# Performance work log

Hardware: AMD Instinct MI355X
Metric: run time of the kernel (lower is better)

Reference implementation:

```python
import jax, jax.numpy as jnp
import numpy as np

C = 512
G = 32  # GroupNorm groups
EPS = 1e-6


def setup_inputs() -> dict:
    key = jax.random.key(0)
    ks = jax.random.split(key, 12)
    B, H, W = 2, 64, 64
    s = 0.02
    return {
        "x": jax.random.normal(ks[0], (B, C, H, W), dtype=jnp.float32),
        "gn_w": jnp.ones((C,), jnp.float32),
        "gn_b": jnp.zeros((C,), jnp.float32),
        "wq": jax.random.normal(ks[1], (C, C), jnp.float32) * s,
        "bq": jnp.zeros((C,), jnp.float32),
        "wk": jax.random.normal(ks[2], (C, C), jnp.float32) * s,
        "bk": jnp.zeros((C,), jnp.float32),
        "wv": jax.random.normal(ks[3], (C, C), jnp.float32) * s,
        "bv": jnp.zeros((C,), jnp.float32),
        "wp": jax.random.normal(ks[4], (C, C), jnp.float32) * s,
        "bp": jnp.zeros((C,), jnp.float32),
    }


def _group_norm(x, w, b):
    B, Cc, H, W = x.shape
    xg = x.reshape(B, G, Cc // G, H, W)
    mu = jnp.mean(xg, axis=(2, 3, 4), keepdims=True)
    var = jnp.var(xg, axis=(2, 3, 4), keepdims=True)
    xn = ((xg - mu) * jax.lax.rsqrt(var + EPS)).reshape(B, Cc, H, W)
    return xn * w[None, :, None, None] + b[None, :, None, None]


def reference(x, gn_w, gn_b, wq, bq, wk, bk, wv, bv, wp, bp):
    B, Cc, H, W = x.shape
    N = H * W
    h = _group_norm(x, gn_w, gn_b)
    hf = h.reshape(B, Cc, N)  # [B,C,N]
    # 1x1 conv == per-position linear over channels
    q = jnp.einsum('dc,bcn->bdn', wq, hf) + bq[None, :, None]
    k = jnp.einsum('dc,bcn->bdn', wk, hf) + bk[None, :, None]
    v = jnp.einsum('dc,bcn->bdn', wv, hf) + bv[None, :, None]
    scale = float(Cc) ** -0.5
    # scores[b,q_pos,k_pos]
    w_ = jnp.einsum('bcq,bck->bqk', q, k) * scale
    w_ = jax.nn.softmax(w_, axis=2)
    # h_[b,c,q] = sum_k v[b,c,k] * w_[b,q,k]
    o = jnp.einsum('bck,bqk->bcq', v, w_)
    o = jnp.einsum('dc,bcn->bdn', wp, o) + bp[None, :, None]
    return x + o.reshape(B, Cc, H, W)
```

## Files before the change

### kernel.cpp

```cpp
#include <hip/hip_runtime.h>


typedef unsigned short u16;
typedef unsigned int u32;
typedef unsigned char u8;
typedef float f32x4 __attribute__((ext_vector_type(4)));

#define NPOS 4096
#define CCH 512

__device__ __forceinline__ u16 f2bf(float f) {
  u32 u = __builtin_bit_cast(u32, f);
  u += 0x7fffu + ((u >> 16) & 1u);
  return (u16)(u >> 16);
}
__device__ __forceinline__ float bf2f(u16 h) {
  u32 u = ((u32)h) << 16;
  return __builtin_bit_cast(float, u);
}
__device__ __forceinline__ u8 f2fp8(float f) {
  u32 pk = __builtin_amdgcn_cvt_pk_fp8_f32(f, f, 0, false);
  return (u8)(pk & 0xff);
}

__device__ __forceinline__ void load16_lds8(const u8* g, u8* l) {
  __builtin_amdgcn_global_load_lds(
      (const __attribute__((address_space(1))) void*)g,
      (__attribute__((address_space(3))) void*)l, 16, 0, 0);
}

__global__ __launch_bounds__(256) void gn_stats_part(const float* __restrict__ x,
                                                     float2* __restrict__ part) {
  int id = blockIdx.x;
  const float4* p = (const float4*)(x + (size_t)id * 16384);
  float s = 0.f, s2 = 0.f;
  for (int i = threadIdx.x; i < 4096; i += 256) {
    float4 u = p[i];
    s += u.x + u.y + u.z + u.w;
    s2 += u.x * u.x + u.y * u.y + u.z * u.z + u.w * u.w;
  }
  for (int o = 32; o; o >>= 1) {
    s += __shfl_xor(s, o);
    s2 += __shfl_xor(s2, o);
  }
  __shared__ float rs[4], rq[4];
  int lane = threadIdx.x & 63, w = threadIdx.x >> 6;
  if (lane == 0) { rs[w] = s; rq[w] = s2; }
  __syncthreads();
  if (threadIdx.x == 0)
    part[id] = make_float2(rs[0] + rs[1] + rs[2] + rs[3], rq[0] + rq[1] + rq[2] + rq[3]);
}

__global__ __launch_bounds__(256) void gn_apply8(const float* __restrict__ x,
                                                 const float* __restrict__ gnw,
                                                 const float* __restrict__ gnb,
                                                 const float2* __restrict__ pstats,
                                                 u8* __restrict__ h8) {
  int b = blockIdx.z, c0 = blockIdx.y * 64, n0 = blockIdx.x * 64;
  __shared__ u8 lt[64][80];
  const float* xb = x + (size_t)b * CCH * NPOS;
  int tid = threadIdx.x;
#pragma unroll
  for (int it = 0; it < 4; ++it) {
    int ci = (tid >> 4) + it * 16;
    int nj = (tid & 15) * 4;
    int c = c0 + ci;
    float4 v = *(const float4*)&xb[(size_t)c * NPOS + n0 + nj];
    const float2* pp = pstats + ((size_t)b * 32 + (c >> 4)) * 4;
    float s = pp[0].x + pp[1].x + pp[2].x + pp[3].x;
    float s2 = pp[0].y + pp[1].y + pp[2].y + pp[3].y;
    float mu = s * (1.f / 65536.f);
    float var = s2 * (1.f / 65536.f) - mu * mu;
    float rst = rsqrtf(var + 1e-6f);
    float w = gnw[c] * rst;
    float bb = gnb[c] - mu * w;
    lt[nj + 0][ci] = f2fp8(v.x * w + bb);
    lt[nj + 1][ci] = f2fp8(v.y * w + bb);
    lt[nj + 2][ci] = f2fp8(v.z * w + bb);
    lt[nj + 3][ci] = f2fp8(v.w * w + bb);
  }
  __syncthreads();
  int ni = tid >> 2, cj = (tid & 3) * 16;
  uint4 o = *(const uint4*)&lt[ni][cj];
  *(uint4*)&h8[((size_t)b * NPOS + n0 + ni) * CCH + c0 + cj] = o;
}

__global__ __launch_bounds__(256) void wconv8(const float* __restrict__ w0,
                                              const float* __restrict__ w1,
                                              const float* __restrict__ w2,
                                              const float* __restrict__ w3,
                                              u8* __restrict__ dst,
                                              const float* __restrict__ bq,
                                              const float* __restrict__ bk,
                                              const float* __restrict__ bv,
                                              float* __restrict__ bqkv) {
  int which = blockIdx.y;
  int bx = blockIdx.x;
  int t = threadIdx.x;
  if (bx == 256) {
    if (which < 3) {
      const float* bsrc = which == 0 ? bq : which == 1 ? bk : bv;
      bqkv[which * 512 + t] = bsrc[t];
      bqkv[which * 512 + 256 + t] = bsrc[256 + t];
    }
    return;
  }
  const float* src = which == 0 ? w0 : which == 1 ? w1 : which == 2 ? w2 : w3;
  u8* d = dst + (size_t)which * (CCH * CCH);
  int i = bx * 256 + t;
  float4 v = ((const float4*)src)[i];
  u32 pk = __builtin_amdgcn_cvt_pk_fp8_f32(v.x, v.y, 0, false);
  pk = __builtin_amdgcn_cvt_pk_fp8_f32(v.z, v.w, pk, true);
  ((u32*)d)[i] = pk;
}

template <int EPI, bool SWIZ>
__global__ __launch_bounds__(256, 4) void gemm_f8(const u8* __restrict__ A,
                                                  const u8* __restrict__ Bm,
                                                  void* __restrict__ Cv,
                                                  const float* __restrict__ bias,
                                                  const float* __restrict__ resid,
                                                  float* __restrict__ lpart,
                                                  float alpha, int K,
                                                  int lda, int ldb, int ldc,
                                                  long sA, long sB, long sC, long sR) {
  const int b = blockIdx.z;
  int bx = blockIdx.x, by = blockIdx.y;
  if (SWIZ) {
    int id = by * gridDim.x + bx;
    int g = id >> 8;
    int w = id & 255;
    bx = (g << 3) | (w & 7);
    by = w >> 3;
  }
  A += (size_t)b * sA;
  Bm += (size_t)b * sB;
  const int m0 = by * 128, n0 = bx * 128;
  __shared__ u8 sAt[128 * 128];
  __shared__ u8 sBt[128 * 128];
  const int tid = threadIdx.x, wave = tid >> 6, lane = tid & 63;
  const int lrow = lane & 15, kch = lane >> 4;
  const int wm = (wave >> 1) * 64, wn = (wave & 1) * 64;
  const int srow = lane >> 3;
  const int sseg = ((lane & 7) ^ srow) * 16;
  f32x4 acc[4][4] = {};

  for (int k0 = 0; k0 < K; k0 += 128) {
#pragma unroll
    for (int r = 0; r < 4; ++r) {
      int ch = wave * 4 + r;
      load16_lds8(A + (size_t)(m0 + ch * 8 + srow) * lda + (k0 + sseg), sAt + ch * 1024);
      load16_lds8(Bm + (size_t)(n0 + ch * 8 + srow) * ldb + (k0 + sseg), sBt + ch * 1024);
    }
    __syncthreads();
#pragma unroll
    for (int kk = 0; kk < 4; ++kk) {
      const int seg16 = kk * 2 + (kch >> 1);
      const int sub = (kch & 1) * 8;
      long af[4], bf[4];
#pragma unroll
      for (int i = 0; i < 4; ++i) {
        int ra = wm + i * 16 + lrow;
        af[i] = *(const long*)(sAt + ra * 128 + (seg16 ^ (ra & 7)) * 16 + sub);
        int rb = wn + i * 16 + lrow;
        bf[i] = *(const long*)(sBt + rb * 128 + (seg16 ^ (rb & 7)) * 16 + sub);
      }
#pragma unroll
      for (int i = 0; i < 4; ++i)
#pragma unroll
        for (int j = 0; j < 4; ++j)
          acc[i][j] =
              __builtin_amdgcn_mfma_f32_16x16x32_fp8_fp8(af[i], bf[j], acc[i][j], 0, 0, 0);
    }
    __syncthreads();
  }

  const int col = lane & 15, rbase = (lane >> 4) * 4;
  const size_t cb = (size_t)b * sC;
  float rsum[4][4];
  if (EPI == 2) {
#pragma unroll
    for (int i = 0; i < 4; ++i)
#pragma unroll
      for (int r = 0; r < 4; ++r) rsum[i][r] = 0.f;
  }
#pragma unroll
  for (int i = 0; i < 4; ++i) {
    int mrow = m0 + wm + i * 16 + rbase;
#pragma unroll
    for (int j = 0; j < 4; ++j) {
      int ncol = n0 + wn + j * 16 + col;
      float bcol = (EPI == 0) ? bias[ncol] : 0.f;
#pragma unroll
      for (int r = 0; r < 4; ++r) {
        int m = mrow + r;
        size_t ci = cb + (size_t)m * ldc + ncol;
        float v = acc[i][j][r];
        if (EPI == 0) {
          ((u8*)Cv)[ci] = f2fp8(v + bcol);
        } else if (EPI == 1) {
          v = v * alpha + bias[m] + resid[(size_t)b * sR + (size_t)m * ldc + ncol];
          ((float*)Cv)[ci] = v;
        } else {
          float s = fminf(fmaxf(v * alpha, -10.f), 4.5f);
          float e = __expf(s);
          rsum[i][r] += e;
          ((u8*)Cv)[ci] = f2fp8(4.f * e);
        }
      }
    }
  }
  if (EPI == 2) {
#pragma unroll
    for (int i = 0; i < 4; ++i) {
#pragma unroll
      for (int r = 0; r < 4; ++r) {
        float v = rsum[i][r];
        v += __shfl_xor(v, 1);
        v += __shfl_xor(v, 2);
        v += __shfl_xor(v, 4);
        v += __shfl_xor(v, 8);
        if ((lane & 15) == 0) {
          int m = m0 + wm + i * 16 + rbase + r;
          lpart[((size_t)b * NPOS + m) * 64 + bx * 2 + (wave & 1)] = v;
        }
      }
    }
  }
}

__global__ __launch_bounds__(256, 4) void gemm_pv_fp8(const u8* __restrict__ Um,
                                                      const u8* __restrict__ Vm,
                                                      u16* __restrict__ part,
                                                      const float* __restrict__ lpart,
                                                      float* __restrict__ lsum) {
  const int b = blockIdx.z >> 2, slice = blockIdx.z & 3;
  const int id = blockIdx.x + (blockIdx.y << 2);
  const int xcd = id & 7, j = id >> 3;
  const int bx = j & 3, by = xcd + ((j >> 2) << 3);
  const u8* A = Um + (size_t)b * ((size_t)NPOS * NPOS) + (size_t)slice * 1024;
  const u8* Bv = Vm + (size_t)b * (CCH * NPOS) + (size_t)slice * 1024;
  const int m0 = by * 128, n0 = bx * 128;
  __shared__ u8 sA[128 * 128];
  __shared__ u8 sB[128 * 128];
  const int tid = threadIdx.x, wave = tid >> 6, lane = tid & 63;
  const int lrow = lane & 15, kch = lane >> 4;
  const int wm = (wave >> 1) * 64, wn = (wave & 1) * 64;
  const int srow = lane >> 3;
  const int sseg = ((lane & 7) ^ srow) * 16;
  f32x4 acc[4][4] = {};

  for (int k0 = 0; k0 < 1024; k0 += 128) {
#pragma unroll
    for (int r = 0; r < 4; ++r) {
      int ch = wave * 4 + r;
      load16_lds8(A + (size_t)(m0 + ch * 8 + srow) * NPOS + (k0 + sseg), sA + ch * 1024);
      load16_lds8(Bv + (size_t)(n0 + ch * 8 + srow) * NPOS + (k0 + sseg), sB + ch * 1024);
    }
    __syncthreads();
#pragma unroll
    for (int kk = 0; kk < 4; ++kk) {
      const int seg16 = kk * 2 + (kch >> 1);
      const int sub = (kch & 1) * 8;
      long af[4], bf[4];
#pragma unroll
      for (int i = 0; i < 4; ++i) {
        int ra = wm + i * 16 + lrow;
        af[i] = *(const long*)(sA + ra * 128 + (seg16 ^ (ra & 7)) * 16 + sub);
        int rb = wn + i * 16 + lrow;
        bf[i] = *(const long*)(sB + rb * 128 + (seg16 ^ (rb & 7)) * 16 + sub);
      }
#pragma unroll
      for (int i = 0; i < 4; ++i)
#pragma unroll
        for (int jj = 0; jj < 4; ++jj)
          acc[i][jj] =
              __builtin_amdgcn_mfma_f32_16x16x32_fp8_fp8(af[i], bf[jj], acc[i][jj], 0, 0, 0);
    }
    __syncthreads();
  }

  const int col = lane & 15, rbase = (lane >> 4) * 4;
  u16* dst = part + (size_t)slice * ((size_t)2 * NPOS * CCH) + (size_t)b * (NPOS * CCH);
#pragma unroll
  for (int i = 0; i < 4; ++i) {
    int mrow = m0 + wm + i * 16 + rbase;
#pragma unroll
    for (int jj = 0; jj < 4; ++jj) {
      int ncol = n0 + wn + jj * 16 + col;
#pragma unroll
      for (int r = 0; r < 4; ++r)
        dst[(size_t)(mrow + r) * CCH + ncol] = f2bf(acc[i][jj][r]);
    }
  }
  if (bx == 0 && tid < 128) {
    const float* lp = lpart + ((size_t)b * NPOS + m0 + tid) * 64;
    float s = 0.f;
#pragma unroll
    for (int c = 0; c < 64; ++c) s += lp[c];
    lsum[(size_t)b * NPOS + m0 + tid] = s;
  }
}

__global__ __launch_bounds__(256) void merge_pv8(const u16* __restrict__ part,
                                                 const float* __restrict__ lsum,
                                                 u8* __restrict__ dst) {
  const long sl = 4194304;
  int i = blockIdx.x * 256 + threadIdx.x;
  long e0 = (long)i * 8;
  int q = (int)((e0 >> 9) & 4095);
  int b = (int)(e0 >> 21);
  float inv = 8.f / lsum[(size_t)b * NPOS + q];
  uint4 a = ((const uint4*)part)[i];
  uint4 bb = ((const uint4*)(part + sl))[i];
  uint4 c = ((const uint4*)(part + 2 * sl))[i];
  uint4 d = ((const uint4*)(part + 3 * sl))[i];
  u32 wa[4] = {a.x, a.y, a.z, a.w}, wb_[4] = {bb.x, bb.y, bb.z, bb.w};
  u32 wc[4] = {c.x, c.y, c.z, c.w}, wd[4] = {d.x, d.y, d.z, d.w};
  float v[8];
#pragma unroll
  for (int j = 0; j < 4; ++j) {
    v[2 * j] = (bf2f((u16)(wa[j] & 0xffff)) + bf2f((u16)(wb_[j] & 0xffff)) +
                bf2f((u16)(wc[j] & 0xffff)) + bf2f((u16)(wd[j] & 0xffff))) * inv;
    v[2 * j + 1] = (bf2f((u16)(wa[j] >> 16)) + bf2f((u16)(wb_[j] >> 16)) +
                    bf2f((u16)(wc[j] >> 16)) + bf2f((u16)(wd[j] >> 16))) * inv;
  }
  uint2 o;
  u32 p0 = __builtin_amdgcn_cvt_pk_fp8_f32(v[0], v[1], 0, false);
  p0 = __builtin_amdgcn_cvt_pk_fp8_f32(v[2], v[3], p0, true);
  u32 p1 = __builtin_amdgcn_cvt_pk_fp8_f32(v[4], v[5], 0, false);
  p1 = __builtin_amdgcn_cvt_pk_fp8_f32(v[6], v[7], p1, true);
  o.x = p0;
  o.y = p1;
  ((uint2*)dst)[i] = o;
}

__global__ __launch_bounds__(256) void transpose_v8(const u8* __restrict__ src,
                                                    u8* __restrict__ dst, int srcld) {
  int b = blockIdx.z, n0 = blockIdx.x * 64, d0 = blockIdx.y * 64;
  __shared__ u8 lt[64][80];
  const u8* s = src + (size_t)b * NPOS * srcld;
  u8* d = dst + (size_t)b * CCH * NPOS;
  int t = threadIdx.x;
  {
    int r = t >> 2, c16 = (t & 3) * 16;
    uint4 v = *(const uint4*)&s[(size_t)(n0 + r) * srcld + d0 + c16];
    *(uint4*)&lt[r][c16] = v;
  }
  __syncthreads();
  {
    int dr = t >> 2, c16 = (t & 3) * 16;
    u8 tmp[16];
#pragma unroll
    for (int j = 0; j < 16; ++j) tmp[j] = lt[c16 + j][dr];
    *(uint4*)&d[(size_t)(d0 + dr) * NPOS + n0 + c16] = *(uint4*)tmp;
  }
}

extern "C" void kernel_launch(void* const* d_in, const int* in_sizes, int n_in,
                              void* d_out, int out_size, void* d_ws, size_t ws_size,
                              hipStream_t stream) {
  const float* x = (const float*)d_in[0];
  const float* gnw = (const float*)d_in[1];
  const float* gnb = (const float*)d_in[2];
  const float* wq = (const float*)d_in[3];
  const float* bq = (const float*)d_in[4];
  const float* wk = (const float*)d_in[5];
  const float* bk = (const float*)d_in[6];
  const float* wv = (const float*)d_in[7];
  const float* bv = (const float*)d_in[8];
  const float* wp = (const float*)d_in[9];
  const float* bp = (const float*)d_in[10];
  float* out = (float*)d_out;

  char* ws = (char*)d_ws;
  size_t off = 0;
  auto alloc = [&](size_t bytes) {
    void* p = ws + off;
    off += (bytes + 1023) & ~(size_t)1023;
    return p;
  };
  float2* pstats = (float2*)alloc(256 * sizeof(float2));
  u8* w8 = (u8*)alloc((size_t)4 * CCH * CCH);
  u8* wp8 = w8 + 3 * CCH * CCH;
  float* bqkv = (float*)alloc(1536 * sizeof(float));
  u8* h8 = (u8*)alloc((size_t)2 * NPOS * CCH);
  u8* qkv8 = (u8*)alloc((size_t)2 * NPOS * 1536);
  u8* v8 = (u8*)alloc((size_t)2 * CCH * NPOS);
  u8* U8 = (u8*)alloc((size_t)2 * NPOS * NPOS);
  float* lpart = (float*)alloc((size_t)2 * NPOS * 64 * 4);
  float* lsum = (float*)alloc((size_t)2 * NPOS * 4);
  u16* part_pv = (u16*)alloc((size_t)4 * 2 * NPOS * CCH * 2);
  u8* o8 = (u8*)alloc((size_t)2 * NPOS * CCH);

  const long sHC8 = (long)NPOS * CCH;
  const long sQKV8 = (long)NPOS * 1536;
  const long sSS8 = (long)NPOS * NPOS;
  const long sOUT = (long)CCH * NPOS;
  const float scale = 0.044194173824159216f;

  gn_stats_part<<<256, 256, 0, stream>>>(x, pstats);
  gn_apply8<<<dim3(64, 8, 2), 256, 0, stream>>>(x, gnw, gnb, pstats, h8);
  wconv8<<<dim3(257, 4), 256, 0, stream>>>(wq, wk, wv, wp, w8, bq, bk, bv, bqkv);
  gemm_f8<0, false><<<dim3(12, 32, 2), 256, 0, stream>>>(
      h8, w8, qkv8, bqkv, nullptr, nullptr, 1.f, CCH, CCH, CCH, 1536,
      sHC8, 0, sQKV8, 0);
  transpose_v8<<<dim3(64, 8, 2), 256, 0, stream>>>(qkv8 + 1024, v8, 1536);
  gemm_f8<2, true><<<dim3(32, 32, 2), 256, 0, stream>>>(
      qkv8, qkv8 + 512, U8, nullptr, nullptr, lpart, scale, CCH, 1536, 1536, NPOS,
      sQKV8, sQKV8, sSS8, 0);
  gemm_pv_fp8<<<dim3(4, 32, 8), 256, 0, stream>>>(U8, v8, part_pv, lpart, lsum);
  merge_pv8<<<2048, 256, 0, stream>>>(part_pv, lsum, o8);
  gemm_f8<1, false><<<dim3(32, 4, 2), 256, 0, stream>>>(
      wp8, o8, out, bp, x, nullptr, 1.f / 32.f, CCH, CCH, CCH, NPOS,
      0, sHC8, sOUT, sOUT);
}
```

Before: 195.6 us.

## Replace QKV, score and PV GEMMs with 256x256 tiled, 4-stage pipelined kernel

Adds a templated 512-thread GEMM with 256x256 output tiles, a 4-deep LDS ring buffer filled by direct-to-LDS loads with explicit vmcnt waits, XCD-aware block remapping and MFMA priority raising. It is used for the QKV projection, the QK^T exp-score GEMM (with lpart now split into 4 column parts per 256 block) and the split-K PV GEMM. This cuts the number of barriers per k-step, raises data reuse per loaded byte and overlaps global loads with MFMA work. In exchange it uses far more registers and LDS per block, which lowers occupancy, and gives fewer blocks for the small QKV GEMM (192 blocks).

Measured after the change: 214.8 us. 9.8% more time.

```diff
diff --git a/kernel.cpp b/kernel.cpp
--- a/kernel.cpp
+++ b/kernel.cpp
@@ -177,13 +177,6 @@
 
   const int col = lane & 15, rbase = (lane >> 4) * 4;
   const size_t cb = (size_t)b * sC;
-  float rsum[4][4];
-  if (EPI == 2) {
-#pragma unroll
-    for (int i = 0; i < 4; ++i)
-#pragma unroll
-      for (int r = 0; r < 4; ++r) rsum[i][r] = 0.f;
-  }
 #pragma unroll
   for (int i = 0; i < 4; ++i) {
     int mrow = m0 + wm + i * 16 + rbase;
@@ -198,107 +191,168 @@
         float v = acc[i][j][r];
         if (EPI == 0) {
           ((u8*)Cv)[ci] = f2fp8(v + bcol);
-        } else if (EPI == 1) {
+        } else {
           v = v * alpha + bias[m] + resid[(size_t)b * sR + (size_t)m * ldc + ncol];
           ((float*)Cv)[ci] = v;
-        } else {
-          float s = fminf(fmaxf(v * alpha, -10.f), 4.5f);
+        }
+      }
+    }
+  }
+}
+
+template <int EPI, int NT>
+__global__ __launch_bounds__(512, 2) void gemm256(
+    const u8* __restrict__ A, const u8* __restrict__ Bm, void* __restrict__ Cv,
+    const float* __restrict__ bias, float* __restrict__ lpart,
+    const float* __restrict__ lpart_in, float* __restrict__ lsum,
+    float alpha, long lda, long ldb, long ldc, long sA, long sB, long sC) {
+  __shared__ u8 LDS[4][32768];
+
+  int lin = blockIdx.x + gridDim.x * blockIdx.y;
+  const int nq = (gridDim.x * gridDim.y) >> 3;
+  lin = (lin & 7) * nq + (lin >> 3);
+  const int bx = lin % gridDim.x, by = lin / gridDim.x;
+  const int m0 = by * 256, n0 = bx * 256;
+
+  int b;
+  const u8 *Ab, *Bb;
+  if constexpr (EPI == 3) {
+    b = blockIdx.z >> 2;
+    const int slice = blockIdx.z & 3;
+    Ab = A + (size_t)b * sA + (size_t)slice * 1024;
+    Bb = Bm + (size_t)b * sB + (size_t)slice * 1024;
+  } else {
+    b = blockIdx.z;
+    Ab = A + (size_t)b * sA;
+    Bb = Bm + (size_t)b * sB;
+  }
+
+  const int tid = threadIdx.x, wave = tid >> 6, lane = tid & 63;
+  const int lrow = lane & 15, kch = lane >> 4;
+  const int wr = wave >> 2, wc = wave & 3;
+
+  const int srow = wave * 16 + (lane >> 2);
+  const int ssw = ((lane & 3) ^ ((srow >> 1) & 3)) * 16;
+  const u8* gA = Ab + (size_t)(m0 + srow) * lda + ssw;
+  const u8* gB = Bb + (size_t)(n0 + srow) * ldb + ssw;
+  u8* lA = &LDS[0][0] + wave * 1024;
+
+  const int swz = (lrow >> 1) & 3;
+  const int cst = (kch & 1) * 8 + (((kch >> 1) ^ swz) << 4);
+  int aoff[8], boff[4];
+#pragma unroll
+  for (int i = 0; i < 8; ++i) aoff[i] = (wr * 128 + i * 16 + lrow) * 64 + cst;
+#pragma unroll
+  for (int j = 0; j < 4; ++j) boff[j] = (wc * 64 + j * 16 + lrow) * 64 + cst + 16384;
+
+  f32x4 acc[8][4] = {};
+
+  auto STAGE = [&](int t) {
+    const int sl = (t & 3) * 32768;
+    const long k0 = (long)t * 64;
+    load16_lds8(gA + k0, lA + sl);
+    load16_lds8(gB + k0, lA + sl + 16384);
+    load16_lds8(gA + 128 * lda + k0, lA + sl + 8192);
+    load16_lds8(gB + 128 * ldb + k0, lA + sl + 24576);
+  };
+
+  STAGE(0);
+  STAGE(1);
+  STAGE(2);
+
+  for (int t = 0; t < NT; ++t) {
+    if (t < NT - 2)
+      asm volatile("s_waitcnt vmcnt(8)" ::: "memory");
+    else if (t == NT - 2)
+      asm volatile("s_waitcnt vmcnt(4)" ::: "memory");
+    else
+      asm volatile("s_waitcnt vmcnt(0)" ::: "memory");
+    asm volatile("s_barrier" ::: "memory");
+    if (t + 3 < NT) STAGE(t + 3);
+    const u8* sb = &LDS[t & 3][0];
+#pragma unroll
+    for (int g = 0; g < 2; ++g) {
+      long a_[8], b_[4];
+#pragma unroll
+      for (int i = 0; i < 8; ++i) a_[i] = *(const long*)(sb + (aoff[i] ^ (g << 5)));
+#pragma unroll
+      for (int j = 0; j < 4; ++j) b_[j] = *(const long*)(sb + (boff[j] ^ (g << 5)));
+      __builtin_amdgcn_s_setprio(1);
+#pragma unroll
+      for (int i = 0; i < 8; ++i)
+#pragma unroll
+        for (int j = 0; j < 4; ++j)
+          acc[i][j] =
+              __builtin_amdgcn_mfma_f32_16x16x32_fp8_fp8(a_[i], b_[j], acc[i][j], 0, 0, 0);
+      __builtin_amdgcn_s_setprio(0);
+    }
+  }
+
+  const int col = lane & 15, rbase = kch * 4;
+  if constexpr (EPI == 0) {
+    u8* C = (u8*)Cv + (size_t)b * sC;
+#pragma unroll
+    for (int i = 0; i < 8; ++i) {
+      const int mrow = m0 + wr * 128 + i * 16 + rbase;
+#pragma unroll
+      for (int j = 0; j < 4; ++j) {
+        const int ncol = n0 + wc * 64 + j * 16 + col;
+        const float bc = bias[ncol];
+#pragma unroll
+        for (int r = 0; r < 4; ++r)
+          C[(size_t)(mrow + r) * ldc + ncol] = f2fp8(acc[i][j][r] + bc);
+      }
+    }
+  } else if constexpr (EPI == 2) {
+    u8* C = (u8*)Cv + (size_t)b * sC;
+#pragma unroll
+    for (int i = 0; i < 8; ++i) {
+      const int mrow = m0 + wr * 128 + i * 16 + rbase;
+      float rsum[4] = {0.f, 0.f, 0.f, 0.f};
+#pragma unroll
+      for (int j = 0; j < 4; ++j) {
+        const int ncol = n0 + wc * 64 + j * 16 + col;
+#pragma unroll
+        for (int r = 0; r < 4; ++r) {
+          float s = fminf(fmaxf(acc[i][j][r] * alpha, -10.f), 4.5f);
           float e = __expf(s);
-          rsum[i][r] += e;
-          ((u8*)Cv)[ci] = f2fp8(4.f * e);
+          rsum[r] += e;
+          C[(size_t)(mrow + r) * ldc + ncol] = f2fp8(4.f * e);
         }
       }
-    }
-  }
-  if (EPI == 2) {
-#pragma unroll
-    for (int i = 0; i < 4; ++i) {
 #pragma unroll
       for (int r = 0; r < 4; ++r) {
-        float v = rsum[i][r];
+        float v = rsum[r];
         v += __shfl_xor(v, 1);
         v += __shfl_xor(v, 2);
         v += __shfl_xor(v, 4);
         v += __shfl_xor(v, 8);
-        if ((lane & 15) == 0) {
-          int m = m0 + wm + i * 16 + rbase + r;
-          lpart[((size_t)b * NPOS + m) * 64 + bx * 2 + (wave & 1)] = v;
-        }
-      }
-    }
-  }
-}
-
-__global__ __launch_bounds__(256, 4) void gemm_pv_fp8(const u8* __restrict__ Um,
-                                                      const u8* __restrict__ Vm,
-                                                      u16* __restrict__ part,
-                                                      const float* __restrict__ lpart,
-                                                      float* __restrict__ lsum) {
-  const int b = blockIdx.z >> 2, slice = blockIdx.z & 3;
-  const int id = blockIdx.x + (blockIdx.y << 2);
-  const int xcd = id & 7, j = id >> 3;
-  const int bx = j & 3, by = xcd + ((j >> 2) << 3);
-  const u8* A = Um + (size_t)b * ((size_t)NPOS * NPOS) + (size_t)slice * 1024;
-  const u8* Bv = Vm + (size_t)b * (CCH * NPOS) + (size_t)slice * 1024;
-  const int m0 = by * 128, n0 = bx * 128;
-  __shared__ u8 sA[128 * 128];
-  __shared__ u8 sB[128 * 128];
-  const int tid = threadIdx.x, wave = tid >> 6, lane = tid & 63;
-  const int lrow = lane & 15, kch = lane >> 4;
-  const int wm = (wave >> 1) * 64, wn = (wave & 1) * 64;
-  const int srow = lane >> 3;
-  const int sseg = ((lane & 7) ^ srow) * 16;
-  f32x4 acc[4][4] = {};
-
-  for (int k0 = 0; k0 < 1024; k0 += 128) {
-#pragma unroll
-    for (int r = 0; r < 4; ++r) {
-      int ch = wave * 4 + r;
-      load16_lds8(A + (size_t)(m0 + ch * 8 + srow) * NPOS + (k0 + sseg), sA + ch * 1024);
-      load16_lds8(Bv + (size_t)(n0 + ch * 8 + srow) * NPOS + (k0 + sseg), sB + ch * 1024);
-    }
-    __syncthreads();
-#pragma unroll
-    for (int kk = 0; kk < 4; ++kk) {
-      const int seg16 = kk * 2 + (kch >> 1);
-      const int sub = (kch & 1) * 8;
-      long af[4], bf[4];
-#pragma unroll
-      for (int i = 0; i < 4; ++i) {
-        int ra = wm + i * 16 + lrow;
-        af[i] = *(const long*)(sA + ra * 128 + (seg16 ^ (ra & 7)) * 16 + sub);
-        int rb = wn + i * 16 + lrow;
-        bf[i] = *(const long*)(sB + rb * 128 + (seg16 ^ (rb & 7)) * 16 + sub);
-      }
-#pragma unroll
-      for (int i = 0; i < 4; ++i)
-#pragma unroll
-        for (int jj = 0; jj < 4; ++jj)
-          acc[i][jj] =
-              __builtin_amdgcn_mfma_f32_16x16x32_fp8_fp8(af[i], bf[jj], acc[i][jj], 0, 0, 0);
-    }
-    __syncthreads();
-  }
-
-  const int col = lane & 15, rbase = (lane >> 4) * 4;
-  u16* dst = part + (size_t)slice * ((size_t)2 * NPOS * CCH) + (size_t)b * (NPOS * CCH);
-#pragma unroll
-  for (int i = 0; i < 4; ++i) {
-    int mrow = m0 + wm + i * 16 + rbase;
-#pragma unroll
-    for (int jj = 0; jj < 4; ++jj) {
-      int ncol = n0 + wn + jj * 16 + col;
-#pragma unroll
-      for (int r = 0; r < 4; ++r)
-        dst[(size_t)(mrow + r) * CCH + ncol] = f2bf(acc[i][jj][r]);
-    }
-  }
-  if (bx == 0 && tid < 128) {
-    const float* lp = lpart + ((size_t)b * NPOS + m0 + tid) * 64;
-    float s = 0.f;
-#pragma unroll
-    for (int c = 0; c < 64; ++c) s += lp[c];
-    lsum[(size_t)b * NPOS + m0 + tid] = s;
+        if (col == 0)
+          lpart[((size_t)b * NPOS + mrow + r) * 64 + bx * 4 + wc] = v;
+      }
+    }
+  } else {
+    const int slice = blockIdx.z & 3;
+    u16* dst = (u16*)Cv + (size_t)slice * ((size_t)2 * NPOS * CCH) +
+               (size_t)b * ((size_t)NPOS * CCH);
+#pragma unroll
+    for (int i = 0; i < 8; ++i) {
+      const int mrow = m0 + wr * 128 + i * 16 + rbase;
+#pragma unroll
+      for (int j = 0; j < 4; ++j) {
+        const int ncol = n0 + wc * 64 + j * 16 + col;
+#pragma unroll
+        for (int r = 0; r < 4; ++r)
+          dst[(size_t)(mrow + r) * CCH + ncol] = f2bf(acc[i][j][r]);
+      }
+    }
+    if (bx == 0 && tid < 256) {
+      const float* lp = lpart_in + ((size_t)b * NPOS + m0 + tid) * 64;
+      float s = 0.f;
+#pragma unroll
+      for (int c = 0; c < 64; ++c) s += lp[c];
+      lsum[(size_t)b * NPOS + m0 + tid] = s;
+    }
   }
 }
 
@@ -402,14 +456,16 @@
   gn_stats_part<<<256, 256, 0, stream>>>(x, pstats);
   gn_apply8<<<dim3(64, 8, 2), 256, 0, stream>>>(x, gnw, gnb, pstats, h8);
   wconv8<<<dim3(257, 4), 256, 0, stream>>>(wq, wk, wv, wp, w8, bq, bk, bv, bqkv);
-  gemm_f8<0, false><<<dim3(12, 32, 2), 256, 0, stream>>>(
-      h8, w8, qkv8, bqkv, nullptr, nullptr, 1.f, CCH, CCH, CCH, 1536,
-      sHC8, 0, sQKV8, 0);
+  gemm256<0, 8><<<dim3(6, 16, 2), 512, 0, stream>>>(
+      h8, w8, qkv8, bqkv, nullptr, nullptr, nullptr, 1.f,
+      CCH, CCH, 1536, sHC8, 0, sQKV8);
   transpose_v8<<<dim3(64, 8, 2), 256, 0, stream>>>(qkv8 + 1024, v8, 1536);
-  gemm_f8<2, true><<<dim3(32, 32, 2), 256, 0, stream>>>(
-      qkv8, qkv8 + 512, U8, nullptr, nullptr, lpart, scale, CCH, 1536, 1536, NPOS,
-      sQKV8, sQKV8, sSS8, 0);
-  gemm_pv_fp8<<<dim3(4, 32, 8), 256, 0, stream>>>(U8, v8, part_pv, lpart, lsum);
+  gemm256<2, 8><<<dim3(16, 16, 2), 512, 0, stream>>>(
+      qkv8, qkv8 + 512, U8, nullptr, lpart, nullptr, nullptr, scale,
+      1536, 1536, NPOS, sQKV8, sQKV8, sSS8);
+  gemm256<3, 16><<<dim3(2, 16, 8), 512, 0, stream>>>(
+      U8, v8, part_pv, nullptr, nullptr, lpart, lsum, 1.f,
+      NPOS, NPOS, CCH, (long)NPOS * NPOS, (long)CCH * NPOS, 0);
   merge_pv8<<<2048, 256, 0, stream>>>(part_pv, lsum, o8);
   gemm_f8<1, false><<<dim3(32, 4, 2), 256, 0, stream>>>(
       wp8, o8, out, bp, x, nullptr, 1.f / 32.f, CCH, CCH, CCH, NPOS,
```

## Triple-buffer LDS with async prefetch in FP8 GEMM kernels

Applied to the files above, without the earlier changes.

Replaces the single-buffered 128-wide K loop in the FP8 GEMM and PV kernels with a three-stage ring of 64-wide K tiles. Global-to-LDS loads for tile t+2 are issued while tile t is computed, and each step ends with one raw waitcnt plus barrier instead of two syncthreads. The aim is to hide global load latency behind MFMA work. The cost is 48KB of LDS per block instead of 32KB, which may limit occupancy. It also relies on hand-tuned vmcnt counts and a new 4-row XOR swizzle layout.

Measured after the change: 228.1 us. 16.6% more time.

```diff
diff --git a/kernel.cpp b/kernel.cpp
--- a/kernel.cpp
+++ b/kernel.cpp
@@ -114,14 +114,14 @@
   ((u32*)d)[i] = pk;
 }
 
-template <int EPI, bool SWIZ>
+template <int EPI, bool SWIZ, int NT>
 __global__ __launch_bounds__(256, 4) void gemm_f8(const u8* __restrict__ A,
                                                   const u8* __restrict__ Bm,
                                                   void* __restrict__ Cv,
                                                   const float* __restrict__ bias,
                                                   const float* __restrict__ resid,
                                                   float* __restrict__ lpart,
-                                                  float alpha, int K,
+                                                  float alpha,
                                                   int lda, int ldb, int ldc,
                                                   long sA, long sB, long sC, long sR) {
   const int b = blockIdx.z;
@@ -136,35 +136,50 @@
   A += (size_t)b * sA;
   Bm += (size_t)b * sB;
   const int m0 = by * 128, n0 = bx * 128;
-  __shared__ u8 sAt[128 * 128];
-  __shared__ u8 sBt[128 * 128];
+  __shared__ u8 L[3][16384];
   const int tid = threadIdx.x, wave = tid >> 6, lane = tid & 63;
   const int lrow = lane & 15, kch = lane >> 4;
   const int wm = (wave >> 1) * 64, wn = (wave & 1) * 64;
-  const int srow = lane >> 3;
-  const int sseg = ((lane & 7) ^ srow) * 16;
+
+  const int sr = lane >> 2;
+  const int ssw = ((lane & 3) ^ (sr & 3)) * 16;
+  const u8* gA0 = A + (size_t)(m0 + wave * 32 + sr) * lda + ssw;
+  const u8* gA1 = gA0 + (size_t)16 * lda;
+  const u8* gB0 = Bm + (size_t)(n0 + wave * 32 + sr) * ldb + ssw;
+  const u8* gB1 = gB0 + (size_t)16 * ldb;
+
+  const int kb = (kch & 1) * 8, ks = kch >> 1;
+  int aoff[4], boff[4];
+#pragma unroll
+  for (int i = 0; i < 4; ++i) {
+    int ra = wm + i * 16 + lrow;
+    aoff[i] = ra * 64 + ((ks ^ (ra & 3)) << 4) + kb;
+  }
+#pragma unroll
+  for (int j = 0; j < 4; ++j) {
+    int rb = wn + j * 16 + lrow;
+    boff[j] = 8192 + rb * 64 + ((ks ^ (rb & 3)) << 4) + kb;
+  }
+
   f32x4 acc[4][4] = {};
 
-  for (int k0 = 0; k0 < K; k0 += 128) {
-#pragma unroll
-    for (int r = 0; r < 4; ++r) {
-      int ch = wave * 4 + r;
-      load16_lds8(A + (size_t)(m0 + ch * 8 + srow) * lda + (k0 + sseg), sAt + ch * 1024);
-      load16_lds8(Bm + (size_t)(n0 + ch * 8 + srow) * ldb + (k0 + sseg), sBt + ch * 1024);
-    }
-    __syncthreads();
-#pragma unroll
-    for (int kk = 0; kk < 4; ++kk) {
-      const int seg16 = kk * 2 + (kch >> 1);
-      const int sub = (kch & 1) * 8;
+  auto STAGE = [&](int t) {
+    u8* d = &L[0][0] + (t % 3) * 16384 + wave * 2048;
+    long ko = (long)t << 6;
+    load16_lds8(gA0 + ko, d);
+    load16_lds8(gA1 + ko, d + 1024);
+    load16_lds8(gB0 + ko, d + 8192);
+    load16_lds8(gB1 + ko, d + 9216);
+  };
+  auto COMP = [&](int t) {
+    const u8* sb = &L[0][0] + (t % 3) * 16384;
+#pragma unroll
+    for (int kk = 0; kk < 2; ++kk) {
       long af[4], bf[4];
 #pragma unroll
-      for (int i = 0; i < 4; ++i) {
-        int ra = wm + i * 16 + lrow;
-        af[i] = *(const long*)(sAt + ra * 128 + (seg16 ^ (ra & 7)) * 16 + sub);
-        int rb = wn + i * 16 + lrow;
-        bf[i] = *(const long*)(sBt + rb * 128 + (seg16 ^ (rb & 7)) * 16 + sub);
-      }
+      for (int i = 0; i < 4; ++i) af[i] = *(const long*)(sb + (aoff[i] ^ (kk << 5)));
+#pragma unroll
+      for (int j = 0; j < 4; ++j) bf[j] = *(const long*)(sb + (boff[j] ^ (kk << 5)));
 #pragma unroll
       for (int i = 0; i < 4; ++i)
 #pragma unroll
@@ -172,8 +187,22 @@
           acc[i][j] =
               __builtin_amdgcn_mfma_f32_16x16x32_fp8_fp8(af[i], bf[j], acc[i][j], 0, 0, 0);
     }
-    __syncthreads();
-  }
+  };
+
+  STAGE(0);
+  STAGE(1);
+  asm volatile("s_waitcnt vmcnt(4) lgkmcnt(0)" ::: "memory");
+  asm volatile("s_barrier" ::: "memory");
+  for (int t = 0; t < NT - 2; ++t) {
+    STAGE(t + 2);
+    COMP(t);
+    asm volatile("s_waitcnt vmcnt(4) lgkmcnt(0)" ::: "memory");
+    asm volatile("s_barrier" ::: "memory");
+  }
+  COMP(NT - 2);
+  asm volatile("s_waitcnt vmcnt(0) lgkmcnt(0)" ::: "memory");
+  asm volatile("s_barrier" ::: "memory");
+  COMP(NT - 1);
 
   const int col = lane & 15, rbase = (lane >> 4) * 4;
   const size_t cb = (size_t)b * sC;
@@ -238,38 +267,53 @@
   const int id = blockIdx.x + (blockIdx.y << 2);
   const int xcd = id & 7, j = id >> 3;
   const int bx = j & 3, by = xcd + ((j >> 2) << 3);
-  const u8* A = Um + (size_t)b * ((size_t)NPOS * NPOS) + (size_t)slice * 1024;
-  const u8* Bv = Vm + (size_t)b * (CCH * NPOS) + (size_t)slice * 1024;
+  const u8* Ab = Um + (size_t)b * ((size_t)NPOS * NPOS) + (size_t)slice * 1024;
+  const u8* Bb = Vm + (size_t)b * (CCH * NPOS) + (size_t)slice * 1024;
   const int m0 = by * 128, n0 = bx * 128;
-  __shared__ u8 sA[128 * 128];
-  __shared__ u8 sB[128 * 128];
+  __shared__ u8 L[3][16384];
   const int tid = threadIdx.x, wave = tid >> 6, lane = tid & 63;
   const int lrow = lane & 15, kch = lane >> 4;
   const int wm = (wave >> 1) * 64, wn = (wave & 1) * 64;
-  const int srow = lane >> 3;
-  const int sseg = ((lane & 7) ^ srow) * 16;
+
+  const int sr = lane >> 2;
+  const int ssw = ((lane & 3) ^ (sr & 3)) * 16;
+  const u8* gA0 = Ab + (size_t)(m0 + wave * 32 + sr) * NPOS + ssw;
+  const u8* gA1 = gA0 + (size_t)16 * NPOS;
+  const u8* gB0 = Bb + (size_t)(n0 + wave * 32 + sr) * NPOS + ssw;
+  const u8* gB1 = gB0 + (size_t)16 * NPOS;
+
+  const int kb = (kch & 1) * 8, ks = kch >> 1;
+  int aoff[4], boff[4];
+#pragma unroll
+  for (int i = 0; i < 4; ++i) {
+    int ra = wm + i * 16 + lrow;
+    aoff[i] = ra * 64 + ((ks ^ (ra & 3)) << 4) + kb;
+  }
+#pragma unroll
+  for (int jj = 0; jj < 4; ++jj) {
+    int rb = wn + jj * 16 + lrow;
+    boff[jj] = 8192 + rb * 64 + ((ks ^ (rb & 3)) << 4) + kb;
+  }
+
   f32x4 acc[4][4] = {};
 
-  for (int k0 = 0; k0 < 1024; k0 += 128) {
-#pragma unroll
-    for (int r = 0; r < 4; ++r) {
-      int ch = wave * 4 + r;
-      load16_lds8(A + (size_t)(m0 + ch * 8 + srow) * NPOS + (k0 + sseg), sA + ch * 1024);
-      load16_lds8(Bv + (size_t)(n0 + ch * 8 + srow) * NPOS + (k0 + sseg), sB + ch * 1024);
-    }
-    __syncthreads();
-#pragma unroll
-    for (int kk = 0; kk < 4; ++kk) {
-      const int seg16 = kk * 2 + (kch >> 1);
-      const int sub = (kch & 1) * 8;
+  auto STAGE = [&](int t) {
+    u8* d = &L[0][0] + (t % 3) * 16384 + wave * 2048;
+    long ko = (long)t << 6;
+    load16_lds8(gA0 + ko, d);
+    load16_lds8(gA1 + ko, d + 1024);
+    load16_lds8(gB0 + ko, d + 8192);
+    load16_lds8(gB1 + ko, d + 9216);
+  };
+  auto COMP = [&](int t) {
+    const u8* sb = &L[0][0] + (t % 3) * 16384;
+#pragma unroll
+    for (int kk = 0; kk < 2; ++kk) {
       long af[4], bf[4];
 #pragma unroll
-      for (int i = 0; i < 4; ++i) {
-        int ra = wm + i * 16 + lrow;
-        af[i] = *(const long*)(sA + ra * 128 + (seg16 ^ (ra & 7)) * 16 + sub);
-        int rb = wn + i * 16 + lrow;
-        bf[i] = *(const long*)(sB + rb * 128 + (seg16 ^ (rb & 7)) * 16 + sub);
-      }
+      for (int i = 0; i < 4; ++i) af[i] = *(const long*)(sb + (aoff[i] ^ (kk << 5)));
+#pragma unroll
+      for (int jj = 0; jj < 4; ++jj) bf[jj] = *(const long*)(sb + (boff[jj] ^ (kk << 5)));
 #pragma unroll
       for (int i = 0; i < 4; ++i)
 #pragma unroll
@@ -277,8 +321,22 @@
           acc[i][jj] =
               __builtin_amdgcn_mfma_f32_16x16x32_fp8_fp8(af[i], bf[jj], acc[i][jj], 0, 0, 0);
     }
-    __syncthreads();
-  }
+  };
+
+  STAGE(0);
+  STAGE(1);
+  asm volatile("s_waitcnt vmcnt(4) lgkmcnt(0)" ::: "memory");
+  asm volatile("s_barrier" ::: "memory");
+  for (int t = 0; t < 14; ++t) {
+    STAGE(t + 2);
+    COMP(t);
+    asm volatile("s_waitcnt vmcnt(4) lgkmcnt(0)" ::: "memory");
+    asm volatile("s_barrier" ::: "memory");
+  }
+  COMP(14);
+  asm volatile("s_waitcnt vmcnt(0) lgkmcnt(0)" ::: "memory");
+  asm volatile("s_barrier" ::: "memory");
+  COMP(15);
 
   const int col = lane & 15, rbase = (lane >> 4) * 4;
   u16* dst = part + (size_t)slice * ((size_t)2 * NPOS * CCH) + (size_t)b * (NPOS * CCH);
@@ -402,16 +460,16 @@
   gn_stats_part<<<256, 256, 0, stream>>>(x, pstats);
   gn_apply8<<<dim3(64, 8, 2), 256, 0, stream>>>(x, gnw, gnb, pstats, h8);
   wconv8<<<dim3(257, 4), 256, 0, stream>>>(wq, wk, wv, wp, w8, bq, bk, bv, bqkv);
-  gemm_f8<0, false><<<dim3(12, 32, 2), 256, 0, stream>>>(
-      h8, w8, qkv8, bqkv, nullptr, nullptr, 1.f, CCH, CCH, CCH, 1536,
+  gemm_f8<0, false, 8><<<dim3(12, 32, 2), 256, 0, stream>>>(
+      h8, w8, qkv8, bqkv, nullptr, nullptr, 1.f, CCH, CCH, 1536,
       sHC8, 0, sQKV8, 0);
   transpose_v8<<<dim3(64, 8, 2), 256, 0, stream>>>(qkv8 + 1024, v8, 1536);
-  gemm_f8<2, true><<<dim3(32, 32, 2), 256, 0, stream>>>(
-      qkv8, qkv8 + 512, U8, nullptr, nullptr, lpart, scale, CCH, 1536, 1536, NPOS,
+  gemm_f8<2, true, 8><<<dim3(32, 32, 2), 256, 0, stream>>>(
+      qkv8, qkv8 + 512, U8, nullptr, nullptr, lpart, scale, 1536, 1536, NPOS,
       sQKV8, sQKV8, sSS8, 0);
   gemm_pv_fp8<<<dim3(4, 32, 8), 256, 0, stream>>>(U8, v8, part_pv, lpart, lsum);
   merge_pv8<<<2048, 256, 0, stream>>>(part_pv, lsum, o8);
-  gemm_f8<1, false><<<dim3(32, 4, 2), 256, 0, stream>>>(
-      wp8, o8, out, bp, x, nullptr, 1.f / 32.f, CCH, CCH, CCH, NPOS,
+  gemm_f8<1, false, 8><<<dim3(32, 4, 2), 256, 0, stream>>>(
+      wp8, o8, out, bp, x, nullptr, 1.f / 32.f, CCH, CCH, NPOS,
       0, sHC8, sOUT, sOUT);
 }
```
